# Kernel optimization log

Measured on AMD Instinct MI355X. Metric: run time of the kernel, lower is better.

## Reference

```python
import jax, jax.numpy as jnp
import numpy as np

NUM_CLASSES = 1000
BATCH = 65536
TEMPERATURE = 1.0
SMOOTHING = 0.1


def setup_inputs() -> dict:
    key = jax.random.key(0)
    k1, k2, k3 = jax.random.split(key, 3)
    x = jax.random.normal(k1, (BATCH, NUM_CLASSES), dtype=jnp.float32)
    class_avg = jax.random.normal(k2, (NUM_CLASSES, NUM_CLASSES), dtype=jnp.float32)
    target = jax.random.randint(k3, (BATCH,), 0, NUM_CLASSES, dtype=jnp.int64)
    return {"x": x, "class_avg": class_avg, "target": target}


def reference(x, class_avg, target):
    C = class_avg.shape[0]
    # class_avg = softmax(class_avg / T) over last dim
    A = jax.nn.softmax(class_avg / TEMPERATURE, axis=-1)  # [C, C]
    # per-class off-diagonal mass: sum over row minus diagonal
    sums = A.sum(axis=-1) - jnp.diagonal(A)  # [C]
    # per-class smoothing matrix S[t, j] = smoothing * (1 - A[t, j]) / sums[t], S[t, t] = 1 - smoothing
    S = SMOOTHING * (1.0 - A) / sums[:, None]  # [C, C]
    diag_idx = jnp.arange(C)
    S = S.at[diag_idx, diag_idx].set(1.0 - SMOOTHING)
    # gather the per-sample smoothing rows (replaces the nested Python loop)
    sm = S[target]  # [B, C]
    logprobs = jax.nn.log_softmax(x, axis=-1)  # [B, C]
    loss = -(logprobs * sm).sum(axis=-1)  # [B]
    return loss.mean()
```

## Files before the change

kernel.cpp:

```cpp
#include <hip/hip_runtime.h>
#include <hip/hip_bf16.h>
#include <math.h>

constexpr int C = 1000;
constexpr int B = 65536;
constexpr float SMOOTH = 0.1f;
constexpr int NBLK = B / 4;

typedef float f4 __attribute__((ext_vector_type(4)));

__device__ inline float wave_reduce_max(float v) {
    #pragma unroll
    for (int off = 32; off > 0; off >>= 1)
        v = fmaxf(v, __shfl_xor(v, off, 64));
    return v;
}
__device__ inline float wave_reduce_sum(float v) {
    #pragma unroll
    for (int off = 32; off > 0; off >>= 1)
        v += __shfl_xor(v, off, 64);
    return v;
}

__device__ inline float block_reduce_max(float v, float* sm) {
    v = wave_reduce_max(v);
    int wave = threadIdx.x >> 6, lane = threadIdx.x & 63;
    if (lane == 0) sm[wave] = v;
    __syncthreads();
    float r = fmaxf(fmaxf(sm[0], sm[1]), fmaxf(sm[2], sm[3]));
    __syncthreads();
    return r;
}
__device__ inline float block_reduce_sum(float v, float* sm) {
    v = wave_reduce_sum(v);
    int wave = threadIdx.x >> 6, lane = threadIdx.x & 63;
    if (lane == 0) sm[wave] = v;
    __syncthreads();
    float r = sm[0] + sm[1] + sm[2] + sm[3];
    __syncthreads();
    return r;
}

__global__ __launch_bounds__(256) void smooth_kernel(
        const float* __restrict__ ca, float* __restrict__ S,
        float* __restrict__ Srow) {
    __shared__ float sm[4];
    __shared__ float diag_sh;
    int t = blockIdx.x;
    int tid = threadIdx.x;
    const float* row = ca + (size_t)t * C;

    float v[4];
    float m = -INFINITY;
    #pragma unroll
    for (int k = 0; k < 4; k++) {
        int j = tid + k * 256;
        v[k] = (j < C) ? row[j] : -INFINITY;
        m = fmaxf(m, v[k]);
    }
    m = block_reduce_max(m, sm);

    float a[4];
    float zl = 0.f;
    #pragma unroll
    for (int k = 0; k < 4; k++) {
        int j = tid + k * 256;
        a[k] = (j < C) ? __expf(v[k] - m) : 0.f;
        zl += a[k];
    }
    float z = block_reduce_sum(zl, sm);
    float inv_z = 1.0f / z;

    float sumA_l = 0.f;
    #pragma unroll
    for (int k = 0; k < 4; k++) {
        a[k] *= inv_z;
        sumA_l += a[k];
        int j = tid + k * 256;
        if (j == t) diag_sh = a[k];
    }
    float sumA = block_reduce_sum(sumA_l, sm);

    float sums = sumA - diag_sh;
    float coef = SMOOTH / sums;
    float* Srt = S + (size_t)t * C;
    float srow_l = 0.f;
    #pragma unroll
    for (int k = 0; k < 4; k++) {
        int j = tid + k * 256;
        if (j < C) {
            float s = (j == t) ? (1.0f - SMOOTH) : (1.0f - a[k]) * coef;
            Srt[j] = s;
            srow_l += s;
        }
    }
    float srow = block_reduce_sum(srow_l, sm);
    if (tid == 0) Srow[t] = srow;
}

__global__ __launch_bounds__(256) void loss_kernel(
        const float* __restrict__ x, const float* __restrict__ S,
        const float* __restrict__ Srow, const int* __restrict__ tgt,
        float* __restrict__ partials) {
    int wave = threadIdx.x >> 6, lane = threadIdx.x & 63;
    int b = blockIdx.x * 4 + wave;

    int t = tgt[b];
    float ss = Srow[t];
    const f4* xr = (const f4*)(x + (size_t)b * C);
    const f4* sr = (const f4*)(S + (size_t)t * C);

    f4 xv[4], sv[4];
    #pragma unroll
    for (int k = 0; k < 3; k++) {
        xv[k] = __builtin_nontemporal_load(xr + lane + k * 64);
        sv[k] = sr[lane + k * 64];
    }
    bool last = (lane + 192) < 250;
    if (last) {
        xv[3] = __builtin_nontemporal_load(xr + lane + 192);
        sv[3] = sr[lane + 192];
    } else {
        xv[3] = f4{-INFINITY, -INFINITY, -INFINITY, -INFINITY};
        sv[3] = f4{0.f, 0.f, 0.f, 0.f};
    }

    float m = -INFINITY;
    #pragma unroll
    for (int k = 0; k < 4; k++)
        m = fmaxf(m, fmaxf(fmaxf(xv[k].x, xv[k].y), fmaxf(xv[k].z, xv[k].w)));
    m = wave_reduce_max(m);

    float zl = 0.f, dl = 0.f;
    #pragma unroll
    for (int k = 0; k < 4; k++) {
        zl += __expf(xv[k].x - m) + __expf(xv[k].y - m) +
              __expf(xv[k].z - m) + __expf(xv[k].w - m);
    }
    #pragma unroll
    for (int k = 0; k < 3; k++) {
        dl = fmaf(sv[k].x, xv[k].x, dl);
        dl = fmaf(sv[k].y, xv[k].y, dl);
        dl = fmaf(sv[k].z, xv[k].z, dl);
        dl = fmaf(sv[k].w, xv[k].w, dl);
    }
    if (last) {
        dl = fmaf(sv[3].x, xv[3].x, dl);
        dl = fmaf(sv[3].y, xv[3].y, dl);
        dl = fmaf(sv[3].z, xv[3].z, dl);
        dl = fmaf(sv[3].w, xv[3].w, dl);
    }
    float z = wave_reduce_sum(zl);
    float d = wave_reduce_sum(dl);
    float lb = (m + __logf(z)) * ss - d;

    __shared__ float wacc[4];
    if (lane == 0) wacc[wave] = lb;
    __syncthreads();
    if (threadIdx.x == 0)
        partials[blockIdx.x] = wacc[0] + wacc[1] + wacc[2] + wacc[3];
}

__global__ __launch_bounds__(256) void reduce_kernel(
        const float* __restrict__ partials, float* __restrict__ out) {
    __shared__ float sm[4];
    const f4* p4 = (const f4*)partials;
    float s = 0.f;
    #pragma unroll
    for (int k = 0; k < 16; k++) {
        f4 v = p4[threadIdx.x + k * 256];
        s += (v.x + v.y) + (v.z + v.w);
    }
    s = block_reduce_sum(s, sm);
    if (threadIdx.x == 0) out[0] = s * (1.0f / (float)B);
}

extern "C" void kernel_launch(void* const* d_in, const int* in_sizes, int n_in,
                              void* d_out, int out_size, void* d_ws, size_t ws_size,
                              hipStream_t stream) {
    const float* x   = (const float*)d_in[0];
    const float* ca  = (const float*)d_in[1];
    const int*   tgt = (const int*)d_in[2];
    float* out = (float*)d_out;

    float* S        = (float*)d_ws;
    float* Srow     = S + (size_t)C * C;
    float* partials = Srow + C;

    smooth_kernel<<<C, 256, 0, stream>>>(ca, S, Srow);
    loss_kernel<<<NBLK, 256, 0, stream>>>(x, S, Srow, tgt, partials);
    reduce_kernel<<<1, 256, 0, stream>>>(partials, out);
}
```

Before: 342.0 us.

## Process two samples per wave in loss kernel and one row per wave in smoothing

The loss kernel now has each wave handle two samples. Their x and S loads are interleaved, the dot product is fused into the load loop, and the max and sum reductions are batched together, all to raise memory-level parallelism and halve the block count. The smoothing kernel assigns one class row per wave with f4 loads and stores, and fetches the diagonal with a shuffle, which removes the block-wide syncs. The nontemporal hint on x loads is dropped, and register pressure rises from holding two rows per wave.

```diff
diff --git a/kernel.cpp b/kernel.cpp
--- a/kernel.cpp
+++ b/kernel.cpp
@@ -1,11 +1,11 @@
 #include <hip/hip_runtime.h>
-#include <hip/hip_bf16.h>
 #include <math.h>
 
 constexpr int C = 1000;
 constexpr int B = 65536;
 constexpr float SMOOTH = 0.1f;
-constexpr int NBLK = B / 4;
+constexpr int SPB = 8;
+constexpr int NBLK = B / SPB;
 
 typedef float f4 __attribute__((ext_vector_type(4)));
 
@@ -21,22 +21,31 @@
         v += __shfl_xor(v, off, 64);
     return v;
 }
-
-__device__ inline float block_reduce_max(float v, float* sm) {
-    v = wave_reduce_max(v);
-    int wave = threadIdx.x >> 6, lane = threadIdx.x & 63;
-    if (lane == 0) sm[wave] = v;
-    __syncthreads();
-    float r = fmaxf(fmaxf(sm[0], sm[1]), fmaxf(sm[2], sm[3]));
-    __syncthreads();
-    return r;
+__device__ inline void wave_reduce_max2(float& a, float& b) {
+    #pragma unroll
+    for (int off = 32; off > 0; off >>= 1) {
+        float ta = __shfl_xor(a, off, 64);
+        float tb = __shfl_xor(b, off, 64);
+        a = fmaxf(a, ta);
+        b = fmaxf(b, tb);
+    }
+}
+__device__ inline void wave_reduce_sum4(float& a, float& b, float& c, float& d) {
+    #pragma unroll
+    for (int off = 32; off > 0; off >>= 1) {
+        float ta = __shfl_xor(a, off, 64);
+        float tb = __shfl_xor(b, off, 64);
+        float tc = __shfl_xor(c, off, 64);
+        float td = __shfl_xor(d, off, 64);
+        a += ta; b += tb; c += tc; d += td;
+    }
 }
 __device__ inline float block_reduce_sum(float v, float* sm) {
     v = wave_reduce_sum(v);
     int wave = threadIdx.x >> 6, lane = threadIdx.x & 63;
     if (lane == 0) sm[wave] = v;
     __syncthreads();
-    float r = sm[0] + sm[1] + sm[2] + sm[3];
+    float r = (sm[0] + sm[1]) + (sm[2] + sm[3]);
     __syncthreads();
     return r;
 }
@@ -44,58 +53,78 @@
 __global__ __launch_bounds__(256) void smooth_kernel(
         const float* __restrict__ ca, float* __restrict__ S,
         float* __restrict__ Srow) {
-    __shared__ float sm[4];
-    __shared__ float diag_sh;
-    int t = blockIdx.x;
-    int tid = threadIdx.x;
-    const float* row = ca + (size_t)t * C;
-
-    float v[4];
+    int wave = threadIdx.x >> 6, lane = threadIdx.x & 63;
+    int t = blockIdx.x * 4 + wave;
+    const f4* row = (const f4*)(ca + (size_t)t * C);
+    bool last = lane < (250 - 192);
+
+    f4 v[4];
+    v[0] = row[lane];
+    v[1] = row[lane + 64];
+    v[2] = row[lane + 128];
+    v[3] = last ? row[lane + 192]
+                : f4{-INFINITY, -INFINITY, -INFINITY, -INFINITY};
+
     float m = -INFINITY;
     #pragma unroll
-    for (int k = 0; k < 4; k++) {
-        int j = tid + k * 256;
-        v[k] = (j < C) ? row[j] : -INFINITY;
-        m = fmaxf(m, v[k]);
-    }
-    m = block_reduce_max(m, sm);
-
-    float a[4];
+    for (int k = 0; k < 4; k++)
+        m = fmaxf(m, fmaxf(fmaxf(v[k].x, v[k].y), fmaxf(v[k].z, v[k].w)));
+    m = wave_reduce_max(m);
+
+    f4 a[4];
     float zl = 0.f;
     #pragma unroll
     for (int k = 0; k < 4; k++) {
-        int j = tid + k * 256;
-        a[k] = (j < C) ? __expf(v[k] - m) : 0.f;
-        zl += a[k];
-    }
-    float z = block_reduce_sum(zl, sm);
+        a[k].x = __expf(v[k].x - m);
+        a[k].y = __expf(v[k].y - m);
+        a[k].z = __expf(v[k].z - m);
+        a[k].w = __expf(v[k].w - m);
+        zl += (a[k].x + a[k].y) + (a[k].z + a[k].w);
+    }
+    float z = wave_reduce_sum(zl);
     float inv_z = 1.0f / z;
 
     float sumA_l = 0.f;
     #pragma unroll
     for (int k = 0; k < 4; k++) {
-        a[k] *= inv_z;
-        sumA_l += a[k];
-        int j = tid + k * 256;
-        if (j == t) diag_sh = a[k];
-    }
-    float sumA = block_reduce_sum(sumA_l, sm);
-
-    float sums = sumA - diag_sh;
+        a[k].x *= inv_z; a[k].y *= inv_z; a[k].z *= inv_z; a[k].w *= inv_z;
+        sumA_l += (a[k].x + a[k].y) + (a[k].z + a[k].w);
+    }
+    float sumA = wave_reduce_sum(sumA_l);
+
+    int q = t >> 2, owner = q & 63, kk = q >> 6, comp = t & 3;
+    f4 av = (kk == 0) ? a[0] : (kk == 1) ? a[1] : (kk == 2) ? a[2] : a[3];
+    float cand = (comp == 0) ? av.x : (comp == 1) ? av.y
+               : (comp == 2) ? av.z : av.w;
+    float diag = __shfl(cand, owner, 64);
+
+    float sums = sumA - diag;
     float coef = SMOOTH / sums;
-    float* Srt = S + (size_t)t * C;
+    f4* Srt = (f4*)(S + (size_t)t * C);
     float srow_l = 0.f;
     #pragma unroll
-    for (int k = 0; k < 4; k++) {
-        int j = tid + k * 256;
-        if (j < C) {
-            float s = (j == t) ? (1.0f - SMOOTH) : (1.0f - a[k]) * coef;
-            Srt[j] = s;
-            srow_l += s;
-        }
-    }
-    float srow = block_reduce_sum(srow_l, sm);
-    if (tid == 0) Srow[t] = srow;
+    for (int k = 0; k < 3; k++) {
+        int jb = (lane + k * 64) * 4;
+        f4 s;
+        s.x = (jb + 0 == t) ? (1.0f - SMOOTH) : (1.0f - a[k].x) * coef;
+        s.y = (jb + 1 == t) ? (1.0f - SMOOTH) : (1.0f - a[k].y) * coef;
+        s.z = (jb + 2 == t) ? (1.0f - SMOOTH) : (1.0f - a[k].z) * coef;
+        s.w = (jb + 3 == t) ? (1.0f - SMOOTH) : (1.0f - a[k].w) * coef;
+        Srt[lane + k * 64] = s;
+        srow_l += (s.x + s.y) + (s.z + s.w);
+    }
+    if (last) {
+        int jb = (lane + 192) * 4;
+        f4 s;
+        s.x = (jb + 0 == t) ? (1.0f - SMOOTH) : (1.0f - a[3].x) * coef;
+        s.y = (jb + 1 == t) ? (1.0f - SMOOTH) : (1.0f - a[3].y) * coef;
+        s.z = (jb + 2 == t) ? (1.0f - SMOOTH) : (1.0f - a[3].z) * coef;
+        s.w = (jb + 3 == t) ? (1.0f - SMOOTH) : (1.0f - a[3].w) * coef;
+        Srt[lane + 192] = s;
+        srow_l += (s.x + s.y) + (s.z + s.w);
+    }
+    float srow = wave_reduce_sum(srow_l);
+    if (lane == 0) Srow[t] = srow;
 }
 
 __global__ __launch_bounds__(256) void loss_kernel(
@@ -103,62 +132,70 @@
         const float* __restrict__ Srow, const int* __restrict__ tgt,
         float* __restrict__ partials) {
     int wave = threadIdx.x >> 6, lane = threadIdx.x & 63;
-    int b = blockIdx.x * 4 + wave;
-
-    int t = tgt[b];
-    float ss = Srow[t];
-    const f4* xr = (const f4*)(x + (size_t)b * C);
-    const f4* sr = (const f4*)(S + (size_t)t * C);
-
-    f4 xv[4], sv[4];
+    int b0 = blockIdx.x * SPB + wave * 2;
+    int b1 = b0 + 1;
+
+    int t0 = tgt[b0], t1 = tgt[b1];
+    float ss0 = Srow[t0], ss1 = Srow[t1];
+    const f4* xr0 = (const f4*)(x + (size_t)b0 * C);
+    const f4* xr1 = (const f4*)(x + (size_t)b1 * C);
+    const f4* sr0 = (const f4*)(S + (size_t)t0 * C);
+    const f4* sr1 = (const f4*)(S + (size_t)t1 * C);
+    bool last = lane < (250 - 192);
+
+    f4 xv0[4], xv1[4];
+    float d0 = 0.f, d1 = 0.f;
     #pragma unroll
     for (int k = 0; k < 3; k++) {
-        xv[k] = __builtin_nontemporal_load(xr + lane + k * 64);
-        sv[k] = sr[lane + k * 64];
-    }
-    bool last = (lane + 192) < 250;
+        xv0[k] = xr0[lane + k * 64];
+        xv1[k] = xr1[lane + k * 64];
+        f4 s0 = sr0[lane + k * 64];
+        f4 s1 = sr1[lane + k * 64];
+        d0 = fmaf(s0.x, xv0[k].x, d0); d0 = fmaf(s0.y, xv0[k].y, d0);
+        d0 = fmaf(s0.z, xv0[k].z, d0); d0 = fmaf(s0.w, xv0[k].w, d0);
+        d1 = fmaf(s1.x, xv1[k].x, d1); d1 = fmaf(s1.y, xv1[k].y, d1);
+        d1 = fmaf(s1.z, xv1[k].z, d1); d1 = fmaf(s1.w, xv1[k].w, d1);
+    }
     if (last) {
-        xv[3] = __builtin_nontemporal_load(xr + lane + 192);
-        sv[3] = sr[lane + 192];
+        xv0[3] = xr0[lane + 192];
+        xv1[3] = xr1[lane + 192];
+        f4 s0 = sr0[lane + 192];
+        f4 s1 = sr1[lane + 192];
+        d0 = fmaf(s0.x, xv0[3].x, d0); d0 = fmaf(s0.y, xv0[3].y, d0);
+        d0 = fmaf(s0.z, xv0[3].z, d0); d0 = fmaf(s0.w, xv0[3].w, d0);
+        d1 = fmaf(s1.x, xv1[3].x, d1); d1 = fmaf(s1.y, xv1[3].y, d1);
+        d1 = fmaf(s1.z, xv1[3].z, d1); d1 = fmaf(s1.w, xv1[3].w, d1);
     } else {
-        xv[3] = f4{-INFINITY, -INFINITY, -INFINITY, -INFINITY};
-        sv[3] = f4{0.f, 0.f, 0.f, 0.f};
-    }
-
-    float m = -INFINITY;
-    #pragma unroll
-    for (int k = 0; k < 4; k++)
-        m = fmaxf(m, fmaxf(fmaxf(xv[k].x, xv[k].y), fmaxf(xv[k].z, xv[k].w)));
-    m = wave_reduce_max(m);
-
-    float zl = 0.f, dl = 0.f;
-    #pragma unroll
-    for (int k = 0; k < 4; k++) {
-        zl += __expf(xv[k].x - m) + __expf(xv[k].y - m) +
-              __expf(xv[k].z - m) + __expf(xv[k].w - m);
-    }
-    #pragma unroll
-    for (int k = 0; k < 3; k++) {
-        dl = fmaf(sv[k].x, xv[k].x, dl);
-        dl = fmaf(sv[k].y, xv[k].y, dl);
-        dl = fmaf(sv[k].z, xv[k].z, dl);
-        dl = fmaf(sv[k].w, xv[k].w, dl);
-    }
-    if (last) {
-        dl = fmaf(sv[3].x, xv[3].x, dl);
-        dl = fmaf(sv[3].y, xv[3].y, dl);
-        dl = fmaf(sv[3].z, xv[3].z, dl);
-        dl = fmaf(sv[3].w, xv[3].w, dl);
-    }
-    float z = wave_reduce_sum(zl);
-    float d = wave_reduce_sum(dl);
-    float lb = (m + __logf(z)) * ss - d;
+        xv0[3] = f4{-INFINITY, -INFINITY, -INFINITY, -INFINITY};
+        xv1[3] = f4{-INFINITY, -INFINITY, -INFINITY, -INFINITY};
+    }
+
+    float m0 = -INFINITY, m1 = -INFINITY;
+    #pragma unroll
+    for (int k = 0; k < 4; k++) {
+        m0 = fmaxf(m0, fmaxf(fmaxf(xv0[k].x, xv0[k].y), fmaxf(xv0[k].z, xv0[k].w)));
+        m1 = fmaxf(m1, fmaxf(fmaxf(xv1[k].x, xv1[k].y), fmaxf(xv1[k].z, xv1[k].w)));
+    }
+    wave_reduce_max2(m0, m1);
+
+    float z0 = 0.f, z1 = 0.f;
+    #pragma unroll
+    for (int k = 0; k < 4; k++) {
+        z0 += __expf(xv0[k].x - m0) + __expf(xv0[k].y - m0) +
+              __expf(xv0[k].z - m0) + __expf(xv0[k].w - m0);
+        z1 += __expf(xv1[k].x - m1) + __expf(xv1[k].y - m1) +
+              __expf(xv1[k].z - m1) + __expf(xv1[k].w - m1);
+    }
+    wave_reduce_sum4(z0, z1, d0, d1);
+
+    float lb0 = (m0 + __logf(z0)) * ss0 - d0;
+    float lb1 = (m1 + __logf(z1)) * ss1 - d1;
 
     __shared__ float wacc[4];
-    if (lane == 0) wacc[wave] = lb;
+    if (lane == 0) wacc[wave] = lb0 + lb1;
     __syncthreads();
     if (threadIdx.x == 0)
-        partials[blockIdx.x] = wacc[0] + wacc[1] + wacc[2] + wacc[3];
+        partials[blockIdx.x] = (wacc[0] + wacc[1]) + (wacc[2] + wacc[3]);
 }
 
 __global__ __launch_bounds__(256) void reduce_kernel(
@@ -167,7 +204,7 @@
     const f4* p4 = (const f4*)partials;
     float s = 0.f;
     #pragma unroll
-    for (int k = 0; k < 16; k++) {
+    for (int k = 0; k < 8; k++) {
         f4 v = p4[threadIdx.x + k * 256];
         s += (v.x + v.y) + (v.z + v.w);
     }
@@ -187,7 +224,7 @@
     float* Srow     = S + (size_t)C * C;
     float* partials = Srow + C;
 
-    smooth_kernel<<<C, 256, 0, stream>>>(ca, S, Srow);
+    smooth_kernel<<<C / 4, 256, 0, stream>>>(ca, S, Srow);
     loss_kernel<<<NBLK, 256, 0, stream>>>(x, S, Srow, tgt, partials);
     reduce_kernel<<<1, 256, 0, stream>>>(partials, out);
 }
```

Result: slower. 357.9 us (+4.7%).
